# Kernel tuning notes

Measured on AMD Instinct MI355X. Metric: run time of the kernel, lower is better.

Reference implementation:

```python
import jax, jax.numpy as jnp
import numpy as np

B, N, F_IN, F_OUT, H = 4, 2048, 128, 256, 4
HD = F_OUT // H


def setup_inputs() -> dict:
    key = jax.random.key(0)
    k1, k2, k3, k4, k5 = jax.random.split(key, 5)
    x = jax.random.normal(k1, (B, N, F_IN), dtype=jnp.float32)
    adj = jax.random.randint(k2, (B, N, N), 0, 2, dtype=jnp.int32)
    # xavier-ish scaled params
    W = jax.random.normal(k3, (F_OUT, F_IN), dtype=jnp.float32) * float(np.sqrt(2.0 / (F_IN + F_OUT)))
    a_l = jax.random.normal(k4, (H, HD), dtype=jnp.float32) * float(np.sqrt(2.0 / (H * HD + 1)))
    a_r = jax.random.normal(k5, (H, HD), dtype=jnp.float32) * float(np.sqrt(2.0 / (H * HD + 1)))
    return {"x": x, "adj": adj, "W": W, "a_l": a_l, "a_r": a_r}


def reference(x, adj, W, a_l, a_r):
    Bb, Nn, _ = x.shape
    h = jnp.einsum('bnf,of->bno', x, W).reshape(Bb, Nn, H, HD)   # [B,N,H,HD]
    e_l = jnp.einsum('bnhd,hd->bnh', h, a_l)                      # [B,N,H]
    e_r = jnp.einsum('bnhd,hd->bnh', h, a_r)                      # [B,N,H]
    e = e_l[:, :, None, :] + e_r[:, None, :, :]                   # [B,N(i),N(j),H]
    e = jax.nn.leaky_relu(e, negative_slope=0.2)
    e = jnp.where(adj[..., None] == 0, -jnp.inf, e)
    alpha = jax.nn.softmax(e, axis=2)                             # softmax over neighbors j
    out = jnp.einsum('bijh,bjhd->bihd', alpha, h)                 # [B,N,H,HD]
    return out.reshape(Bb, Nn, F_OUT)
```

## Files before the change

### kernel.cpp

```cpp
#include <hip/hip_runtime.h>
#include <stdint.h>

#define BB 4
#define NN 2048
#define F_IN 128
#define F_OUT 256
#define NH 4
#define HD 64

typedef float f32x4 __attribute__((ext_vector_type(4)));
typedef float f32x2 __attribute__((ext_vector_type(2)));
typedef short s16x8 __attribute__((ext_vector_type(8)));
typedef int i32x4 __attribute__((ext_vector_type(4)));
typedef unsigned long long u64;
typedef unsigned short u16;

#define LOG2E 1.4426950408889634f

__device__ __forceinline__ u16 f32_to_bf16_rtn(float f) {
    union { float f; uint32_t u; } v; v.f = f;
    uint32_t u = v.u;
    u += 0x7fffu + ((u >> 16) & 1u);
    return (u16)(u >> 16);
}

__device__ __forceinline__ float exp2_fast(float x) {
#if __has_builtin(__builtin_amdgcn_exp2f)
    return __builtin_amdgcn_exp2f(x);
#else
    return exp2f(x);
#endif
}

__device__ __forceinline__ int sbfe1(uint32_t v, int k) {
#if __has_builtin(__builtin_amdgcn_sbfe)
    return __builtin_amdgcn_sbfe((int)v, k, 1);
#else
    return ((int32_t)(v << (31 - k))) >> 31;
#endif
}

__global__ __launch_bounds__(256) void k01(
    const int* __restrict__ adj, const float* __restrict__ x,
    const float* __restrict__ W, const float* __restrict__ a_l,
    const float* __restrict__ a_r, u64* __restrict__ abits,
    u16* __restrict__ hB, float* __restrict__ el, f32x2* __restrict__ er12)
{
    const int t = threadIdx.x;

    __shared__ __align__(16) float xs[16][F_IN];
    __shared__ __align__(16) float red[4 * 64 * 20];

    if (blockIdx.x >= 512) {
        const int wid = ((blockIdx.x - 512) << 2) | (t >> 6);
        const int lane = t & 63;
        const int* rowp = adj + (size_t)wid * NN;
        u64 mym = 0;
        for (int g = 0; g < 4; ++g) {
            int v[8];
#pragma unroll
            for (int u = 0; u < 8; ++u) v[u] = rowp[(g * 8 + u) * 64 + lane];
#pragma unroll
            for (int u = 0; u < 8; ++u) {
                u64 m = __ballot(v[u] != 0);
                if (lane == g * 8 + u) mym = m;
            }
        }
        if (lane < 32) abits[(size_t)wid * 32 + lane] = mym;
        return;
    }

    const int b = blockIdx.x >> 7;
    const int n0 = (blockIdx.x & 127) * 16;

    {
        const f32x4* src = (const f32x4*)(x + ((size_t)b * NN + n0) * F_IN);
        f32x4* dst = (f32x4*)&xs[0][0];
        dst[t] = src[t];
        dst[t + 256] = src[t + 256];
    }
    __syncthreads();

    float acc[16];
#pragma unroll
    for (int n = 0; n < 16; ++n) acc[n] = 0.f;

    const float* wrow = W + (size_t)t * F_IN;
#pragma unroll 2
    for (int k0 = 0; k0 < F_IN; k0 += 8) {
        f32x4 w0 = *(const f32x4*)(wrow + k0);
        f32x4 w1 = *(const f32x4*)(wrow + k0 + 4);
#pragma unroll
        for (int n = 0; n < 16; ++n) {
            f32x4 xa = *(const f32x4*)&xs[n][k0];
            f32x4 xb = *(const f32x4*)&xs[n][k0 + 4];
            float s = acc[n];
            s = fmaf(xa[0], w0[0], s); s = fmaf(xa[1], w0[1], s);
            s = fmaf(xa[2], w0[2], s); s = fmaf(xa[3], w0[3], s);
            s = fmaf(xb[0], w1[0], s); s = fmaf(xb[1], w1[1], s);
            s = fmaf(xb[2], w1[2], s); s = fmaf(xb[3], w1[3], s);
            acc[n] = s;
        }
    }

    const int w = t >> 6, lane = t & 63;
    const float al = a_l[t];
    const float ar = a_r[t];
    const int n_ = lane & 15, og = lane >> 4;
    float sl, sr;
    {
        float* rp = &red[((size_t)w * 64 + lane) * 20];
#pragma unroll
        for (int q = 0; q < 4; ++q) {
            f32x4 v;
#pragma unroll
            for (int e = 0; e < 4; ++e) v[e] = acc[q * 4 + e] * al;
            *(f32x4*)(rp + q * 4) = v;
        }
    }
    __syncthreads();
    {
        float s = 0.f;
#pragma unroll
        for (int oo = 0; oo < 16; ++oo)
            s += red[((size_t)w * 64 + og + 4 * oo) * 20 + n_];
        s += __shfl_xor(s, 16, 64); s += __shfl_xor(s, 32, 64);
        sl = s;
    }
    __syncthreads();
    {
        float* rp = &red[((size_t)w * 64 + lane) * 20];
#pragma unroll
        for (int q = 0; q < 4; ++q) {
            f32x4 v;
#pragma unroll
            for (int e = 0; e < 4; ++e) v[e] = acc[q * 4 + e] * ar;
            *(f32x4*)(rp + q * 4) = v;
        }
    }
    __syncthreads();
    {
        float s = 0.f;
#pragma unroll
        for (int oo = 0; oo < 16; ++oo)
            s += red[((size_t)w * 64 + og + 4 * oo) * 20 + n_];
        s += __shfl_xor(s, 16, 64); s += __shfl_xor(s, 32, 64);
        sr = s;
    }
    if (lane < 16) {
        el[((size_t)b * NH + w) * NN + n0 + lane] = sl * LOG2E;
        float sre = sr * LOG2E;
        f32x2 v2; v2[0] = exp2_fast(sre); v2[1] = exp2_fast(0.2f * sre);
        er12[((size_t)b * NH + w) * NN + n0 + lane] = v2;
    }

    const int dcol = t & 15, cb = (t >> 4) & 3;
    const int jt32 = n0 >> 5;
    const int lb = dcol + ((n0 >> 3) & 2) * 16;
    u16* hb = hB + ((((size_t)b * 64 + jt32) * 4 + w) * 4 + cb) * 512 + (size_t)lb * 8;
    s16x8 pk0, pk1;
#pragma unroll
    for (int n = 0; n < 8; ++n) pk0[n] = (short)f32_to_bf16_rtn(acc[n]);
#pragma unroll
    for (int n = 0; n < 8; ++n) pk1[n] = (short)f32_to_bf16_rtn(acc[n + 8]);
    *(s16x8*)hb         = pk0;
    *(s16x8*)(hb + 128) = pk1;
}

#define MSTRIDE 68

__global__ __launch_bounds__(256, 4) void k2_attn(
    const uint32_t* __restrict__ abits32, const u16* __restrict__ hB,
    const float* __restrict__ el, const f32x2* __restrict__ er12,
    float* __restrict__ out)
{
    __shared__ __align__(16) char smem[33792];
    float*    er_lds   = (float*)smem;
    uint32_t* mask_lds = (uint32_t*)(smem + 16384);
    float*    racc     = (float*)smem;

    const int t = threadIdx.x;
    const int jq = t >> 6, l = t & 63;
    int bid = blockIdx.x;
    bid = (bid & 7) * 128 + (bid >> 3);
    const int b = bid >> 8;
    const int w = (bid >> 6) & 3;
    const int i0 = (bid & 63) * 32;
    const int r = l & 15;
    const int kb = l >> 4;
    const int ks = kb * 8;
    const int irow0 = i0 + r, irow1 = irow0 + 16;

    {
        const f32x4* gsrc = (const f32x4*)(er12 + (size_t)(b * NH + w) * NN);
        f32x4* edst = (f32x4*)er_lds;
#pragma unroll
        for (int p = 0; p < 4; ++p) edst[t + p * 256] = gsrc[t + p * 256];
        const i32x4* msrc = (const i32x4*)(abits32 + ((size_t)b * NN + i0) * 64);
        i32x4 mv0 = msrc[t * 2];
        i32x4 mv1 = msrc[t * 2 + 1];
        const int mrow = t >> 3, mc = (t & 7) * 8;
        *(i32x4*)&mask_lds[mrow * MSTRIDE + mc]     = mv0;
        *(i32x4*)&mask_lds[mrow * MSTRIDE + mc + 4] = mv1;
    }

    const u16* hbp = hB + ((((size_t)b * 64 + jq * 16) * 4 + w) * 4) * 512 + (size_t)l * 8;
    const float eli0 = el[((size_t)b * NH + w) * NN + irow0];
    const float eli1 = el[((size_t)b * NH + w) * NN + irow1];
    const float E1i0 = exp2_fast(eli0), E2i0 = exp2_fast(0.2f * eli0);
    const float E1i1 = exp2_fast(eli1), E2i1 = exp2_fast(0.2f * eli1);

    f32x4 a00 = {0.f,0.f,0.f,0.f}, a01 = a00, a02 = a00, a03 = a00, as0 = a00;
    f32x4 a10 = a00, a11 = a00, a12 = a00, a13 = a00, as1 = a00;
    s16x8 ones;
#pragma unroll
    for (int k = 0; k < 8; ++k) ones[k] = (short)0x3F80;

    s16x8 b0c = *(const s16x8*)(hbp + 0 * 512);
    s16x8 b1c = *(const s16x8*)(hbp + 1 * 512);
    s16x8 b2c = *(const s16x8*)(hbp + 2 * 512);
    s16x8 b3c = *(const s16x8*)(hbp + 3 * 512);
    __syncthreads();

#define MFMA_BF16 __builtin_amdgcn_mfma_f32_16x16x32_bf16
#define BODY(IT, PF)                                                          \
    {                                                                         \
        const int itv = (IT);                                                 \
        const int jb2 = (jq * 512 + itv * 32 + ks) * 2;                       \
        f32x4 e0 = *(const f32x4*)(er_lds + jb2);                             \
        f32x4 e1 = *(const f32x4*)(er_lds + jb2 + 4);                         \
        f32x4 e2 = *(const f32x4*)(er_lds + jb2 + 8);                         \
        f32x4 e3 = *(const f32x4*)(er_lds + jb2 + 12);                        \
        uint32_t w2a = mask_lds[r * MSTRIDE + jq * 16 + itv] >> ks;           \
        uint32_t w2b = mask_lds[(16 + r) * MSTRIDE + jq * 16 + itv] >> ks;    \
        s16x8 b0n, b1n, b2n, b3n;                                             \
        if (PF) {                                                             \
            const u16* hp_ = hbp + (size_t)(itv + 1) * 8192;                  \
            b0n = *(const s16x8*)(hp_ + 0 * 512);                             \
            b1n = *(const s16x8*)(hp_ + 1 * 512);                             \
            b2n = *(const s16x8*)(hp_ + 2 * 512);                             \
            b3n = *(const s16x8*)(hp_ + 3 * 512);                             \
        }                                                                     \
        __builtin_amdgcn_sched_barrier(0);                                    \
        union { s16x8 v; uint32_t u[4]; } afa, afb;                           \
        _Pragma("unroll")                                                     \
        for (int kk = 0; kk < 4; ++kk) {                                      \
            f32x4 ev = (kk == 0) ? e0 : ((kk == 1) ? e1 : ((kk == 2) ? e2 : e3)); \
            float t00 = E1i0 * ev[0], m00 = E2i0 * ev[1];                     \
            float t01 = E1i0 * ev[2], m01 = E2i0 * ev[3];                     \
            float t10 = E1i1 * ev[0], m10 = E2i1 * ev[1];                     \
            float t11 = E1i1 * ev[2], m11 = E2i1 * ev[3];                     \
            float p00 = (t00 >= 1.0f) ? t00 : m00;                            \
            float p01 = (t01 >= 1.0f) ? t01 : m01;                            \
            float p10 = (t10 >= 1.0f) ? t10 : m10;                            \
            float p11 = (t11 >= 1.0f) ? t11 : m11;                            \
            union { float f; uint32_t u; } c00, c01, c10, c11;                \
            c00.f = p00; c01.f = p01; c10.f = p10; c11.f = p11;               \
            uint32_t q00 = c00.u & (uint32_t)sbfe1(w2a, 2 * kk);              \
            uint32_t q01 = c01.u & (uint32_t)sbfe1(w2a, 2 * kk + 1);          \
            uint32_t q10 = c10.u & (uint32_t)sbfe1(w2b, 2 * kk);              \
            uint32_t q11 = c11.u & (uint32_t)sbfe1(w2b, 2 * kk + 1);          \
            afa.u[kk] = __builtin_amdgcn_perm(q01, q00, 0x07060302);          \
            afb.u[kk] = __builtin_amdgcn_perm(q11, q10, 0x07060302);          \
        }                                                                     \
        a00 = MFMA_BF16(afa.v, b0c, a00, 0, 0, 0);                            \
        a01 = MFMA_BF16(afa.v, b1c, a01, 0, 0, 0);                            \
        a02 = MFMA_BF16(afa.v, b2c, a02, 0, 0, 0);                            \
        a03 = MFMA_BF16(afa.v, b3c, a03, 0, 0, 0);                            \
        as0 = MFMA_BF16(afa.v, ones, as0, 0, 0, 0);                           \
        a10 = MFMA_BF16(afb.v, b0c, a10, 0, 0, 0);                            \
        a11 = MFMA_BF16(afb.v, b1c, a11, 0, 0, 0);                            \
        a12 = MFMA_BF16(afb.v, b2c, a12, 0, 0, 0);                            \
        a13 = MFMA_BF16(afb.v, b3c, a13, 0, 0, 0);                            \
        as1 = MFMA_BF16(afb.v, ones, as1, 0, 0, 0);                           \
        if (PF) { b0c = b0n; b1c = b1n; b2c = b2n; b3c = b3n; }               \
    }

    for (int g = 0; g < 3; ++g) {
#pragma unroll
        for (int s = 0; s < 4; ++s) BODY(g * 4 + s, 1);
    }
    BODY(12, 1); BODY(13, 1); BODY(14, 1); BODY(15, 0);

    __syncthreads();
    if (jq > 0) {
        float* p = &racc[((jq - 1) * 64 + l) * 44];
        *(f32x4*)(p +  0) = a00; *(f32x4*)(p +  4) = a01;
        *(f32x4*)(p +  8) = a02; *(f32x4*)(p + 12) = a03;
        *(f32x4*)(p + 16) = as0;
        *(f32x4*)(p + 20) = a10; *(f32x4*)(p + 24) = a11;
        *(f32x4*)(p + 28) = a12; *(f32x4*)(p + 32) = a13;
        *(f32x4*)(p + 36) = as1;
    }
    __syncthreads();
    if (jq == 0) {
#pragma unroll
        for (int s = 0; s < 3; ++s) {
            const float* p = &racc[(s * 64 + l) * 44];
            a00 += *(const f32x4*)(p +  0); a01 += *(const f32x4*)(p +  4);
            a02 += *(const f32x4*)(p +  8); a03 += *(const f32x4*)(p + 12);
            as0 += *(const f32x4*)(p + 16);
            a10 += *(const f32x4*)(p + 20); a11 += *(const f32x4*)(p + 24);
            a12 += *(const f32x4*)(p + 28); a13 += *(const f32x4*)(p + 32);
            as1 += *(const f32x4*)(p + 36);
        }

        float* op = out + ((size_t)b * NN + i0) * F_OUT + w * HD;
#pragma unroll
        for (int q = 0; q < 4; ++q) {
            const int row0 = kb * 4 + q;
            float inv0 = 1.0f / as0[q];
            op[(size_t)row0 * F_OUT +  0 + r] = a00[q] * inv0;
            op[(size_t)row0 * F_OUT + 16 + r] = a01[q] * inv0;
            op[(size_t)row0 * F_OUT + 32 + r] = a02[q] * inv0;
            op[(size_t)row0 * F_OUT + 48 + r] = a03[q] * inv0;
            const int row1 = 16 + kb * 4 + q;
            float inv1 = 1.0f / as1[q];
            op[(size_t)row1 * F_OUT +  0 + r] = a10[q] * inv1;
            op[(size_t)row1 * F_OUT + 16 + r] = a11[q] * inv1;
            op[(size_t)row1 * F_OUT + 32 + r] = a12[q] * inv1;
            op[(size_t)row1 * F_OUT + 48 + r] = a13[q] * inv1;
        }
    }
}

extern "C" void kernel_launch(void* const* d_in, const int* in_sizes, int n_in,
                              void* d_out, int out_size, void* d_ws, size_t ws_size,
                              hipStream_t stream) {
    const float* x   = (const float*)d_in[0];
    const int*   adj = (const int*)d_in[1];
    const float* W   = (const float*)d_in[2];
    const float* a_l = (const float*)d_in[3];
    const float* a_r = (const float*)d_in[4];
    float* out = (float*)d_out;

    char* ws = (char*)d_ws;
    u16*   hB    = (u16*)ws;
    u64*   abits = (u64*)(ws + (size_t)BB * F_OUT * NN * 2);
    float* el    = (float*)(ws + (size_t)BB * F_OUT * NN * 2 + (size_t)BB * NN * 32 * 8);
    f32x2* er12  = (f32x2*)(el + (size_t)BB * NH * NN);

    k01<<<512 + BB * NN / 4, 256, 0, stream>>>(adj, x, W, a_l, a_r, abits, hB, el, er12);
    k2_attn<<<BB * NH * (NN / 32), 256, 0, stream>>>((const uint32_t*)abits, hB, el, er12, out);
}
```

Measured before the change: 49.01 us.

## Alias LDS, nontemporal adj loads/out stores, remap blocks, use fmaxf for leaky-relu

The projection kernel now aliases the x tile onto the reduction buffer to cut LDS use, adding a barrier before reuse. Adjacency loads and output stores use nontemporal hints to avoid polluting caches. The attention kernel lowers its occupancy hint from 4 to 3 blocks per SIMD, changes the block-to-(batch, head, row) mapping, and replaces the compare-select leaky-relu with fmaxf on the exponentials. These are several unrelated tweaks that trade register pressure, cache behaviour and scheduling against each other.

```diff
diff --git a/kernel.cpp b/kernel.cpp
--- a/kernel.cpp
+++ b/kernel.cpp
@@ -48,8 +48,8 @@
 {
     const int t = threadIdx.x;
 
-    __shared__ __align__(16) float xs[16][F_IN];
     __shared__ __align__(16) float red[4 * 64 * 20];
+    float (*xs)[F_IN] = (float(*)[F_IN])red;
 
     if (blockIdx.x >= 512) {
         const int wid = ((blockIdx.x - 512) << 2) | (t >> 6);
@@ -59,7 +59,8 @@
         for (int g = 0; g < 4; ++g) {
             int v[8];
 #pragma unroll
-            for (int u = 0; u < 8; ++u) v[u] = rowp[(g * 8 + u) * 64 + lane];
+            for (int u = 0; u < 8; ++u)
+                v[u] = __builtin_nontemporal_load(rowp + (g * 8 + u) * 64 + lane);
 #pragma unroll
             for (int u = 0; u < 8; ++u) {
                 u64 m = __ballot(v[u] != 0);
@@ -102,6 +103,7 @@
             acc[n] = s;
         }
     }
+    __syncthreads();
 
     const int w = t >> 6, lane = t & 63;
     const float al = a_l[t];
@@ -169,7 +171,7 @@
 
 #define MSTRIDE 68
 
-__global__ __launch_bounds__(256, 4) void k2_attn(
+__global__ __launch_bounds__(256, 3) void k2_attn(
     const uint32_t* __restrict__ abits32, const u16* __restrict__ hB,
     const float* __restrict__ el, const f32x2* __restrict__ er12,
     float* __restrict__ out)
@@ -181,11 +183,12 @@
 
     const int t = threadIdx.x;
     const int jq = t >> 6, l = t & 63;
-    int bid = blockIdx.x;
-    bid = (bid & 7) * 128 + (bid >> 3);
-    const int b = bid >> 8;
-    const int w = (bid >> 6) & 3;
-    const int i0 = (bid & 63) * 32;
+    const int o = blockIdx.x;
+    const int kblk = o >> 3;
+    const int bw = (o & 7) + 8 * (kblk & 1);
+    const int b = bw >> 2;
+    const int w = bw & 3;
+    const int i0 = (kblk >> 1) * 32;
     const int r = l & 15;
     const int kb = l >> 4;
     const int ks = kb * 8;
@@ -250,10 +253,10 @@
             float t01 = E1i0 * ev[2], m01 = E2i0 * ev[3];                     \
             float t10 = E1i1 * ev[0], m10 = E2i1 * ev[1];                     \
             float t11 = E1i1 * ev[2], m11 = E2i1 * ev[3];                     \
-            float p00 = (t00 >= 1.0f) ? t00 : m00;                            \
-            float p01 = (t01 >= 1.0f) ? t01 : m01;                            \
-            float p10 = (t10 >= 1.0f) ? t10 : m10;                            \
-            float p11 = (t11 >= 1.0f) ? t11 : m11;                            \
+            float p00 = fmaxf(t00, m00);           \
+            float p01 = fmaxf(t01, m01);                                      \
+            float p10 = fmaxf(t10, m10);                                      \
+            float p11 = fmaxf(t11, m11);                                      \
             union { float f; uint32_t u; } c00, c01, c10, c11;                \
             c00.f = p00; c01.f = p01; c10.f = p10; c11.f = p11;               \
             uint32_t q00 = c00.u & (uint32_t)sbfe1(w2a, 2 * kk);              \
@@ -310,16 +313,16 @@
         for (int q = 0; q < 4; ++q) {
             const int row0 = kb * 4 + q;
             float inv0 = 1.0f / as0[q];
-            op[(size_t)row0 * F_OUT +  0 + r] = a00[q] * inv0;
-            op[(size_t)row0 * F_OUT + 16 + r] = a01[q] * inv0;
-            op[(size_t)row0 * F_OUT + 32 + r] = a02[q] * inv0;
-            op[(size_t)row0 * F_OUT + 48 + r] = a03[q] * inv0;
+            __builtin_nontemporal_store(a00[q] * inv0, &op[(size_t)row0 * F_OUT +  0 + r]);
+            __builtin_nontemporal_store(a01[q] * inv0, &op[(size_t)row0 * F_OUT + 16 + r]);
+            __builtin_nontemporal_store(a02[q] * inv0, &op[(size_t)row0 * F_OUT + 32 + r]);
+            __builtin_nontemporal_store(a03[q] * inv0, &op[(size_t)row0 * F_OUT + 48 + r]);
             const int row1 = 16 + kb * 4 + q;
             float inv1 = 1.0f / as1[q];
-            op[(size_t)row1 * F_OUT +  0 + r] = a10[q] * inv1;
-            op[(size_t)row1 * F_OUT + 16 + r] = a11[q] * inv1;
-            op[(size_t)row1 * F_OUT + 32 + r] = a12[q] * inv1;
-            op[(size_t)row1 * F_OUT + 48 + r] = a13[q] * inv1;
+            __builtin_nontemporal_store(a10[q] * inv1, &op[(size_t)row1 * F_OUT +  0 + r]);
+            __builtin_nontemporal_store(a11[q] * inv1, &op[(size_t)row1 * F_OUT + 16 + r]);
+            __builtin_nontemporal_store(a12[q] * inv1, &op[(size_t)row1 * F_OUT + 32 + r]);
+            __builtin_nontemporal_store(a13[q] * inv1, &op[(size_t)row1 * F_OUT + 48 + r]);
         }
     }
 }
```

Measured after the change: 46.19 us. -5.7%, faster.
